# Performance work log

Hardware: AMD Instinct MI355X
Metric: run time of the kernel (lower is better)

## Reference

```python
import jax, jax.numpy as jnp
import numpy as np

WINDOW = 128
LOOK_BACKWARD = 1
LOOK_FORWARD = 1
SCALE = 64 ** -0.5  # dim_heads ** -0.5 per LocalAttention(dim=dim_heads)


def look_around(x, pad_value):
    # x: (b, w, WINDOW, ...). Pad window axis, concat shifted copies along axis 2.
    w = x.shape[1]
    pad_width = [(0, 0)] * x.ndim
    pad_width[1] = (LOOK_BACKWARD, LOOK_FORWARD)
    padded = jnp.pad(x, pad_width, constant_values=pad_value)
    return jnp.concatenate([padded[:, i:i + w] for i in range(LOOK_BACKWARD + LOOK_FORWARD + 1)], axis=2)


def setup_inputs() -> dict:
    key = jax.random.key(0)
    ks = jax.random.split(key, 8)
    B, N, D_IN, D_QK = 8, 4000, 512, 512
    return {
        "queries": jax.random.normal(ks[0], (B, N, D_IN), jnp.float32),
        "keys": jax.random.normal(ks[1], (B, N, D_IN), jnp.float32),
        "values": jax.random.normal(ks[2], (B, N, D_IN), jnp.float32),
        "mask": jax.random.bernoulli(ks[3], 0.9, (B, N)),
        "w_q": jax.random.normal(ks[4], (D_QK, D_IN), jnp.float32) / np.sqrt(D_IN).astype(np.float32),
        "b_q": jnp.zeros((D_QK,), jnp.float32),
        "w_k": jax.random.normal(ks[5], (D_QK, D_IN), jnp.float32) / np.sqrt(D_IN).astype(np.float32),
        "b_k": jnp.zeros((D_QK,), jnp.float32),
        "w_v": jax.random.normal(ks[6], (D_QK, D_IN), jnp.float32) / np.sqrt(D_IN).astype(np.float32),
        "b_v": jnp.zeros((D_QK,), jnp.float32),
    }


def local_attention(q, k, v, mask):
    b, n, d = q.shape
    pad = (-n) % WINDOW  # autopad=True
    npad = n + pad
    q = jnp.pad(q, ((0, 0), (0, pad), (0, 0)))
    k = jnp.pad(k, ((0, 0), (0, pad), (0, 0)))
    v = jnp.pad(v, ((0, 0), (0, pad), (0, 0)))
    m = jnp.pad(mask, ((0, 0), (0, pad)), constant_values=False)
    w = npad // WINDOW
    bq = q.reshape(b, w, WINDOW, d) * SCALE
    bk = look_around(k.reshape(b, w, WINDOW, d), 0.0)   # (b, w, 3W, d)
    bv = look_around(v.reshape(b, w, WINDOW, d), 0.0)
    sim = jnp.einsum('bwie,bwje->bwij', bq, bk)          # (b, w, W, 3W)
    seq = jnp.arange(npad).reshape(1, w, WINDOW)
    bq_k = look_around(seq, -1)                          # (1, w, 3W)
    pad_mask = (bq_k == -1)[:, :, None, :]
    key_mask = look_around(m.reshape(b, w, WINDOW), False)[:, :, None, :]
    neg = -jnp.finfo(sim.dtype).max
    sim = jnp.where(pad_mask | (~key_mask), neg, sim)
    attn = jax.nn.softmax(sim, axis=-1)
    out = jnp.einsum('bwij,bwje->bwie', attn, bv)
    return out.reshape(b, npad, d)[:, :n]


def reference(queries, keys, values, mask, w_q, b_q, w_k, b_k, w_v, b_v):
    q = queries @ w_q.T + b_q
    k = keys @ w_k.T + b_k
    v = values @ w_v.T + b_v
    return local_attention(q, k, v, mask)
```

## Files before the change

### kernel.cpp

```cpp
#include <hip/hip_runtime.h>
#include <cstdint>
#include <cstddef>

#define NB    8
#define NSEQ  4000
#define NPAD  4096
#define DIM   512
#define NWIN  32
#define SCALE 0.125f
#define NEG_MAX (-3.402823466e38f)

typedef _Float16 half8 __attribute__((ext_vector_type(8)));
typedef _Float16 half4 __attribute__((ext_vector_type(4)));
typedef float    floatx4 __attribute__((ext_vector_type(4)));

typedef const __attribute__((address_space(1))) void* gas_p;
typedef __attribute__((address_space(3))) void*       las_p;

__device__ __forceinline__ void gl_lds16(const void* g, void* l) {
    __builtin_amdgcn_global_load_lds((gas_p)g, (las_p)l, 16, 0, 0);
}

__global__ __launch_bounds__(256) void convert_w(
    const float* __restrict__ wq, const float* __restrict__ wk,
    const float* __restrict__ wv, _Float16* __restrict__ wh)
{
    int i = (blockIdx.x * 256 + threadIdx.x) * 4;
    floatx4 a = *(const floatx4*)(wq + i);
    half4 h;
    #pragma unroll
    for (int j = 0; j < 4; j++) h[j] = (_Float16)(a[j] * SCALE);
    *(half4*)(wh + i) = h;

    a = *(const floatx4*)(wk + i);
    #pragma unroll
    for (int j = 0; j < 4; j++) h[j] = (_Float16)a[j];
    *(half4*)(wh + 262144 + i) = h;

    a = *(const floatx4*)(wv + i);
    #pragma unroll
    for (int j = 0; j < 4; j++) h[j] = (_Float16)a[j];
    *(half4*)(wh + 524288 + i) = h;
}

__global__ __launch_bounds__(256) void proj_gemm(
    const float* __restrict__ xq, const float* __restrict__ xk,
    const float* __restrict__ xv, const _Float16* __restrict__ wh,
    const float* __restrict__ bq, const float* __restrict__ bk,
    const float* __restrict__ bv,
    _Float16* __restrict__ qh, _Float16* __restrict__ kh,
    _Float16* __restrict__ vT)
{
    const int z  = blockIdx.z;
    const int m0 = blockIdx.x * 128;
    const int n0 = blockIdx.y * 128;
    const int tid = threadIdx.x;
    const int wid = tid >> 6, lane = tid & 63;
    const int l16 = lane & 15, lg = lane >> 4;
    const int wr = wid >> 1, wc = wid & 1;

    __shared__ __align__(16) _Float16 AB[2][2][4096];

    const float* X = (z == 0) ? xq : ((z == 1) ? xk : xv);
    const _Float16* Wz = wh + (size_t)z * DIM * DIM;

    const int s0 = tid * 16;
    const int s1 = 4096 + tid * 16;
    const int k8_0 = s0 >> 11, row_0 = (s0 >> 4) & 127;
    const int k8_1 = s1 >> 11, row_1 = (s1 >> 4) & 127;
    const int ldsu0 = wid * 1024;
    const int ldsu1 = 4096 + wid * 1024;

    const float* xp0 = X + (size_t)(m0 + row_0) * DIM + k8_0 * 8;
    const float* xp1 = X + (size_t)(m0 + row_1) * DIM + k8_1 * 8;

    floatx4 acc[4][4];
    #pragma unroll
    for (int m = 0; m < 4; m++)
        #pragma unroll
        for (int n = 0; n < 4; n++) acc[m][n] = floatx4{0.f, 0.f, 0.f, 0.f};

    {
        floatx4 a0 = *(const floatx4*)(xp0);
        floatx4 a1 = *(const floatx4*)(xp0 + 4);
        floatx4 a2 = *(const floatx4*)(xp1);
        floatx4 a3 = *(const floatx4*)(xp1 + 4);
        gl_lds16(Wz + (size_t)(n0 + row_0) * DIM + k8_0 * 8, (char*)&AB[0][1][0] + ldsu0);
        gl_lds16(Wz + (size_t)(n0 + row_1) * DIM + k8_1 * 8, (char*)&AB[0][1][0] + ldsu1);
        half8 h0, h1;
        #pragma unroll
        for (int j = 0; j < 4; j++) {
            h0[j] = (_Float16)a0[j]; h0[j + 4] = (_Float16)a1[j];
            h1[j] = (_Float16)a2[j]; h1[j + 4] = (_Float16)a3[j];
        }
        *(half8*)((char*)&AB[0][0][0] + s0) = h0;
        *(half8*)((char*)&AB[0][0][0] + s1) = h1;
    }
    __syncthreads();

    for (int ks = 0; ks < 16; ks++) {
        const int cur = ks & 1;
        floatx4 a0, a1, a2, a3;
        if (ks < 15) {
            const int k0 = (ks + 1) * 32;
            a0 = *(const floatx4*)(xp0 + k0);
            a1 = *(const floatx4*)(xp0 + k0 + 4);
            a2 = *(const floatx4*)(xp1 + k0);
            a3 = *(const floatx4*)(xp1 + k0 + 4);
            gl_lds16(Wz + (size_t)(n0 + row_0) * DIM + k0 + k8_0 * 8,
                     (char*)&AB[cur ^ 1][1][0] + ldsu0);
            gl_lds16(Wz + (size_t)(n0 + row_1) * DIM + k0 + k8_1 * 8,
                     (char*)&AB[cur ^ 1][1][0] + ldsu1);
        }
        const _Float16* Ar = &AB[cur][0][lg * 1024 + (wr * 64 + l16) * 8];
        const _Float16* Br = &AB[cur][1][lg * 1024 + (wc * 64 + l16) * 8];
        half8 af[4], bf[4];
        #pragma unroll
        for (int m = 0; m < 4; m++) af[m] = *(const half8*)(Ar + m * 128);
        #pragma unroll
        for (int n = 0; n < 4; n++) bf[n] = *(const half8*)(Br + n * 128);
        #pragma unroll
        for (int m = 0; m < 4; m++)
            #pragma unroll
            for (int n = 0; n < 4; n++)
                acc[m][n] = __builtin_amdgcn_mfma_f32_16x16x32_f16(af[m], bf[n], acc[m][n], 0, 0, 0);
        if (ks < 15) {
            half8 h0, h1;
            #pragma unroll
            for (int j = 0; j < 4; j++) {
                h0[j] = (_Float16)a0[j]; h0[j + 4] = (_Float16)a1[j];
                h1[j] = (_Float16)a2[j]; h1[j + 4] = (_Float16)a3[j];
            }
            *(half8*)((char*)&AB[cur ^ 1][0][0] + s0) = h0;
            *(half8*)((char*)&AB[cur ^ 1][0][0] + s1) = h1;
            __syncthreads();
        }
    }

    const float* bias = (z == 0) ? bq : ((z == 1) ? bk : bv);
    const float bscale = (z == 0) ? SCALE : 1.0f;
    #pragma unroll
    for (int n = 0; n < 4; n++) {
        const int ncol = n0 + wc * 64 + n * 16 + l16;
        const float bn = bias[ncol] * bscale;
        #pragma unroll
        for (int m = 0; m < 4; m++) {
            const int r0 = m0 + wr * 64 + m * 16 + lg * 4;
            const int bb = r0 / NSEQ;
            const int i0 = r0 - bb * NSEQ;
            if (z < 2) {
                _Float16* O = (z == 0) ? qh : kh;
                #pragma unroll
                for (int j = 0; j < 4; j++)
                    O[((size_t)(bb * NPAD + i0 + j)) * DIM + ncol] = (_Float16)(acc[m][n][j] + bn);
            } else {
                half4 pk;
                #pragma unroll
                for (int j = 0; j < 4; j++) pk[j] = (_Float16)(acc[m][n][j] + bn);
                *(half4*)(vT + ((size_t)(bb * DIM + ncol)) * NPAD + i0) = pk;
            }
        }
    }
}

__global__ __launch_bounds__(256) void attn_scores(
    const _Float16* __restrict__ qh, const _Float16* __restrict__ kh,
    const int* __restrict__ mask, _Float16* __restrict__ P)
{
    const int h = blockIdx.x, w = blockIdx.y, b = blockIdx.z;
    const int tid = threadIdx.x;
    const int wid = tid >> 6, lane = tid & 63;
    const int l16 = lane & 15, lg = lane >> 4;

    __shared__ __align__(16) _Float16 Kl[2][12288];

    const int kbase = w * 128 - 128;
    const _Float16* khb = kh + (size_t)b * NPAD * DIM;

    int srcoff[6], ldsoff[6];
    #pragma unroll
    for (int c = 0; c < 6; c++) {
        int s = c * 4096 + tid * 16;
        int k8 = s / 6144;
        int key = (s - k8 * 6144) >> 4;
        int g = kbase + key;
        int gc = g < 0 ? 0 : (g > NPAD - 1 ? NPAD - 1 : g);
        srcoff[c] = gc * DIM + k8 * 8;
        ldsoff[c] = c * 4096 + wid * 1024;
    }

#define STAGE_K2(bb, k0) do {                                                   \
    _Pragma("unroll")                                                           \
    for (int c = 0; c < 6; c++)                                                 \
        gl_lds16(khb + (size_t)srcoff[c] + (k0), (char*)&Kl[bb][0] + ldsoff[c]);\
} while (0)

    const int qr0 = w * 128 + h * 64 + wid * 16;
    const _Float16* qrow = qh + ((size_t)(b * NPAD + qr0 + l16)) * DIM + lg * 8;

    floatx4 acc[24];
    #pragma unroll
    for (int t = 0; t < 24; t++) acc[t] = floatx4{0.f, 0.f, 0.f, 0.f};

    half8 qcur = *(const half8*)(qrow);
    STAGE_K2(0, 0);
    __syncthreads();
    for (int ks = 0; ks < 16; ks++) {
        const int cur = ks & 1;
        half8 qnext;
        if (ks < 15) {
            STAGE_K2(cur ^ 1, (ks + 1) * 32);
            qnext = *(const half8*)(qrow + (ks + 1) * 32);
        }
        const _Float16* Kb = &Kl[cur][lg * 3072 + l16 * 8];
        #pragma unroll
        for (int t = 0; t < 24; t++) {
            half8 bf = *(const half8*)(Kb + t * 128);
            acc[t] = __builtin_amdgcn_mfma_f32_16x16x32_f16(qcur, bf, acc[t], 0, 0, 0);
        }
        if (ks < 15) { __syncthreads(); qcur = qnext; }
    }
#undef STAGE_K2

    const int* mb = mask + b * NSEQ;
    #pragma unroll
    for (int t = 0; t < 24; t++) {
        int g = kbase + t * 16 + l16;
        bool keep = (g >= 0) && (g < NSEQ) && (mb[(g >= 0 && g < NSEQ) ? g : 0] != 0);
        if (!keep) acc[t] = floatx4{NEG_MAX, NEG_MAX, NEG_MAX, NEG_MAX};
    }

    _Float16* Pw = P + ((size_t)(b * NWIN + w)) * 128 * 384
                     + (size_t)(h * 64 + wid * 16) * 384;
    #pragma unroll
    for (int j = 0; j < 4; j++) {
        float mj = NEG_MAX;
        #pragma unroll
        for (int t = 0; t < 24; t++) mj = fmaxf(mj, acc[t][j]);
        mj = fmaxf(mj, __shfl_xor(mj, 1));
        mj = fmaxf(mj, __shfl_xor(mj, 2));
        mj = fmaxf(mj, __shfl_xor(mj, 4));
        mj = fmaxf(mj, __shfl_xor(mj, 8));

        float p[24];
        float lsum = 0.f;
        #pragma unroll
        for (int t = 0; t < 24; t++) { p[t] = __expf(acc[t][j] - mj); lsum += p[t]; }
        lsum += __shfl_xor(lsum, 1);
        lsum += __shfl_xor(lsum, 2);
        lsum += __shfl_xor(lsum, 4);
        lsum += __shfl_xor(lsum, 8);
        float rinv = 1.0f / lsum;

        int r = lg * 4 + j;
        #pragma unroll
        for (int t = 0; t < 24; t++)
            Pw[(size_t)r * 384 + t * 16 + l16] = (_Float16)(p[t] * rinv);
    }
}

__global__ __launch_bounds__(256) void attn_pv(
    const _Float16* __restrict__ P, const _Float16* __restrict__ vT,
    float* __restrict__ out)
{
    const int dq = blockIdx.x, w = blockIdx.y, b = blockIdx.z;
    const int tid = threadIdx.x;
    const int wid = tid >> 6, lane = tid & 63;
    const int l16 = lane & 15, lg = lane >> 4;
    const int d0 = dq * 128;

    __shared__ __align__(16) _Float16 Pl[2][4096];
    __shared__ __align__(16) _Float16 Vl[2][4096];

    const _Float16* Pw = P + ((size_t)(b * NWIN + w)) * 128 * 384;
    const _Float16* vb = vT + (size_t)b * DIM * NPAD;
    const int iw_base = w * 128 - 128;

    const int s0 = tid * 16;
    const int s1 = 4096 + tid * 16;
    const int k8_0 = s0 >> 11, row_0 = (s0 >> 4) & 127;
    const int k8_1 = s1 >> 11, row_1 = (s1 >> 4) & 127;
    const int ldsu0 = wid * 1024;
    const int ldsu1 = 4096 + wid * 1024;

#define STAGE_K3(bb, ks) do {                                                   \
    int i0 = (ks) * 32;                                                         \
    gl_lds16(Pw + (size_t)row_0 * 384 + i0 + k8_0 * 8, (char*)&Pl[bb][0] + ldsu0);\
    gl_lds16(Pw + (size_t)row_1 * 384 + i0 + k8_1 * 8, (char*)&Pl[bb][0] + ldsu1);\
    int ig0 = iw_base + i0 + k8_0 * 8;                                          \
    ig0 = ig0 < 0 ? 0 : (ig0 > NPAD - 8 ? NPAD - 8 : ig0);                      \
    int ig1 = iw_base + i0 + k8_1 * 8;                                          \
    ig1 = ig1 < 0 ? 0 : (ig1 > NPAD - 8 ? NPAD - 8 : ig1);                      \
    gl_lds16(vb + (size_t)(d0 + row_0) * NPAD + ig0, (char*)&Vl[bb][0] + ldsu0);\
    gl_lds16(vb + (size_t)(d0 + row_1) * NPAD + ig1, (char*)&Vl[bb][0] + ldsu1);\
} while (0)

    floatx4 acc[2][8];
    #pragma unroll
    for (int m = 0; m < 2; m++)
        #pragma unroll
        for (int n = 0; n < 8; n++) acc[m][n] = floatx4{0.f, 0.f, 0.f, 0.f};

    STAGE_K3(0, 0);
    __syncthreads();
    for (int ks = 0; ks < 12; ks++) {
        const int cur = ks & 1;
        if (ks < 11) STAGE_K3(cur ^ 1, ks + 1);
        const _Float16* Pr = &Pl[cur][lg * 1024 + (wid * 32 + l16) * 8];
        const _Float16* Vr = &Vl[cur][lg * 1024 + l16 * 8];
        half8 pa[2], vf[8];
        #pragma unroll
        for (int m = 0; m < 2; m++) pa[m] = *(const half8*)(Pr + m * 128);
        #pragma unroll
        for (int n = 0; n < 8; n++) vf[n] = *(const half8*)(Vr + n * 128);
        #pragma unroll
        for (int m = 0; m < 2; m++)
            #pragma unroll
            for (int n = 0; n < 8; n++)
                acc[m][n] = __builtin_amdgcn_mfma_f32_16x16x32_f16(pa[m], vf[n], acc[m][n], 0, 0, 0);
        if (ks < 11) __syncthreads();
    }
#undef STAGE_K3

    #pragma unroll
    for (int m = 0; m < 2; m++) {
        #pragma unroll
        for (int j = 0; j < 4; j++) {
            int i = w * 128 + wid * 32 + m * 16 + lg * 4 + j;
            if (i < NSEQ) {
                float* orow = out + ((size_t)b * NSEQ + i) * DIM + d0;
                #pragma unroll
                for (int n = 0; n < 8; n++) orow[n * 16 + l16] = acc[m][n][j];
            }
        }
    }
}

extern "C" void kernel_launch(void* const* d_in, const int* in_sizes, int n_in,
                              void* d_out, int out_size, void* d_ws, size_t ws_size,
                              hipStream_t stream)
{
    const float* xq = (const float*)d_in[0];
    const float* xk = (const float*)d_in[1];
    const float* xv = (const float*)d_in[2];
    const int*  msk = (const int*)d_in[3];
    const float* wq = (const float*)d_in[4];
    const float* bq = (const float*)d_in[5];
    const float* wk = (const float*)d_in[6];
    const float* bk = (const float*)d_in[7];
    const float* wv = (const float*)d_in[8];
    const float* bv = (const float*)d_in[9];

    _Float16* qh = (_Float16*)d_ws;
    _Float16* kh = qh + (size_t)NB * NPAD * DIM;
    _Float16* vT = kh + (size_t)NB * NPAD * DIM;
    _Float16* wh = vT + (size_t)NB * NPAD * DIM;
    _Float16* P  = wh + (size_t)3 * DIM * DIM;
    float* out = (float*)d_out;

    convert_w<<<dim3(256), dim3(256), 0, stream>>>(wq, wk, wv, wh);
    proj_gemm<<<dim3(250, 4, 3), dim3(256), 0, stream>>>(
        xq, xk, xv, wh, bq, bk, bv, qh, kh, vT);
    attn_scores<<<dim3(2, NWIN, NB), dim3(256), 0, stream>>>(qh, kh, msk, P);
    attn_pv<<<dim3(4, NWIN, NB), dim3(256), 0, stream>>>(P, vT, out);
}
```

Baseline: 469.8 us.

## Fuse attention scores and PV into one kernel; remap projection grid for XCD locality

Merges the score/softmax kernel and the P·V kernel into one. Probabilities now stay in LDS, written with an XOR swizzle and reused from the K staging buffer, so the global round trip through the P workspace and one launch go away. The PV stage now reads V straight from global memory with no LDS staging or double buffering, and each block computes all 512 output columns using 32 accumulators. That raises register pressure and adds uncoalesced loads. Separately, the projection GEMM grid is flattened and remapped so that consecutive block IDs across the 8 XCDs cover the same row tiles, aiming for better L2 reuse of activations.

After: 511.6 us. +8.9%, slower.

```diff
diff --git a/kernel.cpp b/kernel.cpp
--- a/kernel.cpp
+++ b/kernel.cpp
@@ -51,9 +51,14 @@
     _Float16* __restrict__ qh, _Float16* __restrict__ kh,
     _Float16* __restrict__ vT)
 {
-    const int z  = blockIdx.z;
-    const int m0 = blockIdx.x * 128;
-    const int n0 = blockIdx.y * 128;
+    const int g = blockIdx.x;
+    const int x = g & 7, s = g >> 3;
+    const int pair = x * 94 + (s >> 2);
+    if (pair >= 750) return;
+    const int z   = pair / 250;
+    const int m0  = (pair - z * 250) * 128;
+    const int n0  = (s & 3) * 128;
+
     const int tid = threadIdx.x;
     const int wid = tid >> 6, lane = tid & 63;
     const int l16 = lane & 15, lg = lane >> 4;
@@ -163,9 +168,10 @@
     }
 }
 
-__global__ __launch_bounds__(256) void attn_scores(
+__global__ __launch_bounds__(256) void attn_fused(
     const _Float16* __restrict__ qh, const _Float16* __restrict__ kh,
-    const int* __restrict__ mask, _Float16* __restrict__ P)
+    const _Float16* __restrict__ vT, const int* __restrict__ mask,
+    float* __restrict__ out)
 {
     const int h = blockIdx.x, w = blockIdx.y, b = blockIdx.z;
     const int tid = threadIdx.x;
@@ -173,6 +179,7 @@
     const int l16 = lane & 15, lg = lane >> 4;
 
     __shared__ __align__(16) _Float16 Kl[2][12288];
+    char* Ps = (char*)&Kl[0][0];
 
     const int kbase = w * 128 - 128;
     const _Float16* khb = kh + (size_t)b * NPAD * DIM;
@@ -183,8 +190,8 @@
         int s = c * 4096 + tid * 16;
         int k8 = s / 6144;
         int key = (s - k8 * 6144) >> 4;
-        int g = kbase + key;
-        int gc = g < 0 ? 0 : (g > NPAD - 1 ? NPAD - 1 : g);
+        int gk = kbase + key;
+        int gc = gk < 0 ? 0 : (gk > NPAD - 1 ? NPAD - 1 : gk);
         srcoff[c] = gc * DIM + k8 * 8;
         ldsoff[c] = c * 4096 + wid * 1024;
     }
@@ -225,13 +232,13 @@
     const int* mb = mask + b * NSEQ;
     #pragma unroll
     for (int t = 0; t < 24; t++) {
-        int g = kbase + t * 16 + l16;
-        bool keep = (g >= 0) && (g < NSEQ) && (mb[(g >= 0 && g < NSEQ) ? g : 0] != 0);
+        int gk = kbase + t * 16 + l16;
+        bool keep = (gk >= 0) && (gk < NSEQ) && (mb[(gk >= 0 && gk < NSEQ) ? gk : 0] != 0);
         if (!keep) acc[t] = floatx4{NEG_MAX, NEG_MAX, NEG_MAX, NEG_MAX};
     }
 
-    _Float16* Pw = P + ((size_t)(b * NWIN + w)) * 128 * 384
-                     + (size_t)(h * 64 + wid * 16) * 384;
+    __syncthreads();
+
     #pragma unroll
     for (int j = 0; j < 4; j++) {
         float mj = NEG_MAX;
@@ -252,86 +259,45 @@
         lsum += __shfl_xor(lsum, 8);
         float rinv = 1.0f / lsum;
 
-        int r = lg * 4 + j;
-        #pragma unroll
-        for (int t = 0; t < 24; t++)
-            Pw[(size_t)r * 384 + t * 16 + l16] = (_Float16)(p[t] * rinv);
-    }
-}
-
-__global__ __launch_bounds__(256) void attn_pv(
-    const _Float16* __restrict__ P, const _Float16* __restrict__ vT,
-    float* __restrict__ out)
-{
-    const int dq = blockIdx.x, w = blockIdx.y, b = blockIdx.z;
-    const int tid = threadIdx.x;
-    const int wid = tid >> 6, lane = tid & 63;
-    const int l16 = lane & 15, lg = lane >> 4;
-    const int d0 = dq * 128;
-
-    __shared__ __align__(16) _Float16 Pl[2][4096];
-    __shared__ __align__(16) _Float16 Vl[2][4096];
-
-    const _Float16* Pw = P + ((size_t)(b * NWIN + w)) * 128 * 384;
+        const int q = wid * 16 + lg * 4 + j;
+        const int qswz = (q & 7) << 4;
+        #pragma unroll
+        for (int t = 0; t < 24; t++) {
+            int byte = (q * 768 + (t * 16 + l16) * 2) ^ qswz;
+            *(_Float16*)(Ps + byte) = (_Float16)(p[t] * rinv);
+        }
+    }
+
+    __syncthreads();
+
     const _Float16* vb = vT + (size_t)b * DIM * NPAD;
-    const int iw_base = w * 128 - 128;
-
-    const int s0 = tid * 16;
-    const int s1 = 4096 + tid * 16;
-    const int k8_0 = s0 >> 11, row_0 = (s0 >> 4) & 127;
-    const int k8_1 = s1 >> 11, row_1 = (s1 >> 4) & 127;
-    const int ldsu0 = wid * 1024;
-    const int ldsu1 = 4096 + wid * 1024;
-
-#define STAGE_K3(bb, ks) do {                                                   \
-    int i0 = (ks) * 32;                                                         \
-    gl_lds16(Pw + (size_t)row_0 * 384 + i0 + k8_0 * 8, (char*)&Pl[bb][0] + ldsu0);\
-    gl_lds16(Pw + (size_t)row_1 * 384 + i0 + k8_1 * 8, (char*)&Pl[bb][0] + ldsu1);\
-    int ig0 = iw_base + i0 + k8_0 * 8;                                          \
-    ig0 = ig0 < 0 ? 0 : (ig0 > NPAD - 8 ? NPAD - 8 : ig0);                      \
-    int ig1 = iw_base + i0 + k8_1 * 8;                                          \
-    ig1 = ig1 < 0 ? 0 : (ig1 > NPAD - 8 ? NPAD - 8 : ig1);                      \
-    gl_lds16(vb + (size_t)(d0 + row_0) * NPAD + ig0, (char*)&Vl[bb][0] + ldsu0);\
-    gl_lds16(vb + (size_t)(d0 + row_1) * NPAD + ig1, (char*)&Vl[bb][0] + ldsu1);\
-} while (0)
-
-    floatx4 acc[2][8];
-    #pragma unroll
-    for (int m = 0; m < 2; m++)
-        #pragma unroll
-        for (int n = 0; n < 8; n++) acc[m][n] = floatx4{0.f, 0.f, 0.f, 0.f};
-
-    STAGE_K3(0, 0);
-    __syncthreads();
+    const int iw_base = kbase;
+
+    floatx4 acc2[32];
+    #pragma unroll
+    for (int t = 0; t < 32; t++) acc2[t] = floatx4{0.f, 0.f, 0.f, 0.f};
+
     for (int ks = 0; ks < 12; ks++) {
-        const int cur = ks & 1;
-        if (ks < 11) STAGE_K3(cur ^ 1, ks + 1);
-        const _Float16* Pr = &Pl[cur][lg * 1024 + (wid * 32 + l16) * 8];
-        const _Float16* Vr = &Vl[cur][lg * 1024 + l16 * 8];
-        half8 pa[2], vf[8];
-        #pragma unroll
-        for (int m = 0; m < 2; m++) pa[m] = *(const half8*)(Pr + m * 128);
-        #pragma unroll
-        for (int n = 0; n < 8; n++) vf[n] = *(const half8*)(Vr + n * 128);
-        #pragma unroll
-        for (int m = 0; m < 2; m++)
+        const int q = wid * 16 + l16;
+        const int abyte = (q * 768 + ks * 64 + lg * 16) ^ ((q & 7) << 4);
+        half8 pa = *(const half8*)(Ps + abyte);
+        int ig = iw_base + ks * 32 + lg * 8;
+        ig = ig < 0 ? 0 : (ig > NPAD - 8 ? NPAD - 8 : ig);
+        const _Float16* vrow = vb + ig;
+        #pragma unroll
+        for (int t = 0; t < 32; t++) {
+            half8 vf = *(const half8*)(vrow + (size_t)(t * 16 + l16) * NPAD);
+            acc2[t] = __builtin_amdgcn_mfma_f32_16x16x32_f16(pa, vf, acc2[t], 0, 0, 0);
+        }
+    }
+
+    #pragma unroll
+    for (int j = 0; j < 4; j++) {
+        const int i = w * 128 + h * 64 + wid * 16 + lg * 4 + j;
+        if (i < NSEQ) {
+            float* orow = out + ((size_t)b * NSEQ + i) * DIM;
             #pragma unroll
-            for (int n = 0; n < 8; n++)
-                acc[m][n] = __builtin_amdgcn_mfma_f32_16x16x32_f16(pa[m], vf[n], acc[m][n], 0, 0, 0);
-        if (ks < 11) __syncthreads();
-    }
-#undef STAGE_K3
-
-    #pragma unroll
-    for (int m = 0; m < 2; m++) {
-        #pragma unroll
-        for (int j = 0; j < 4; j++) {
-            int i = w * 128 + wid * 32 + m * 16 + lg * 4 + j;
-            if (i < NSEQ) {
-                float* orow = out + ((size_t)b * NSEQ + i) * DIM + d0;
-                #pragma unroll
-                for (int n = 0; n < 8; n++) orow[n * 16 + l16] = acc[m][n][j];
-            }
+            for (int t = 0; t < 32; t++) orow[t * 16 + l16] = acc2[t][j];
         }
     }
 }
@@ -355,12 +321,10 @@
     _Float16* kh = qh + (size_t)NB * NPAD * DIM;
     _Float16* vT = kh + (size_t)NB * NPAD * DIM;
     _Float16* wh = vT + (size_t)NB * NPAD * DIM;
-    _Float16* P  = wh + (size_t)3 * DIM * DIM;
     float* out = (float*)d_out;
 
     convert_w<<<dim3(256), dim3(256), 0, stream>>>(wq, wk, wv, wh);
-    proj_gemm<<<dim3(250, 4, 3), dim3(256), 0, stream>>>(
+    proj_gemm<<<dim3(3008), dim3(256), 0, stream>>>(
         xq, xk, xv, wh, bq, bk, bv, qh, kh, vT);
-    attn_scores<<<dim3(2, NWIN, NB), dim3(256), 0, stream>>>(qh, kh, msk, P);
-    attn_pv<<<dim3(4, NWIN, NB), dim3(256), 0, stream>>>(P, vT, out);
-}
+    attn_fused<<<dim3(2, NWIN, NB), dim3(256), 0, stream>>>(qh, kh, vT, msk, out);
+}
```

## Replace global-to-LDS direct loads with register staging and remap GEMM blocks per XCD

Applied to the files above, without the earlier changes.

All three matmul kernels drop the direct global_load_lds path. Tiles are now loaded into registers at the top of each k-step and written to the double-buffered LDS after the MFMA work, and the thread-to-row mapping is changed so consecutive threads read contiguous 16-byte chunks of a row. The projection GEMM moves to a 1D grid of 3008 blocks, remapped so that the 4 column tiles sharing one row tile land on the same XCD, aiming for better L2 reuse of the fp32 input rows. The cost is more VGPR pressure and extra ds_write instructions, plus 8 idle blocks in the padded grid.

Result: faster. 393.6 us (-16.2%).

```diff
diff --git a/kernel.cpp b/kernel.cpp
--- a/kernel.cpp
+++ b/kernel.cpp
@@ -14,13 +14,6 @@
 typedef _Float16 half4 __attribute__((ext_vector_type(4)));
 typedef float    floatx4 __attribute__((ext_vector_type(4)));
 
-typedef const __attribute__((address_space(1))) void* gas_p;
-typedef __attribute__((address_space(3))) void*       las_p;
-
-__device__ __forceinline__ void gl_lds16(const void* g, void* l) {
-    __builtin_amdgcn_global_load_lds((gas_p)g, (las_p)l, 16, 0, 0);
-}
-
 __global__ __launch_bounds__(256) void convert_w(
     const float* __restrict__ wq, const float* __restrict__ wk,
     const float* __restrict__ wv, _Float16* __restrict__ wh)
@@ -51,9 +44,14 @@
     _Float16* __restrict__ qh, _Float16* __restrict__ kh,
     _Float16* __restrict__ vT)
 {
-    const int z  = blockIdx.z;
-    const int m0 = blockIdx.x * 128;
-    const int n0 = blockIdx.y * 128;
+    const int g = blockIdx.x;
+    const int x = g & 7, s = g >> 3;
+    const int pair = x * 94 + (s >> 2);
+    if (pair >= 750) return;
+    const int z   = pair / 250;
+    const int m0  = (pair - z * 250) * 128;
+    const int n0  = (s & 3) * 128;
+
     const int tid = threadIdx.x;
     const int wid = tid >> 6, lane = tid & 63;
     const int l16 = lane & 15, lg = lane >> 4;
@@ -64,15 +62,14 @@
     const float* X = (z == 0) ? xq : ((z == 1) ? xk : xv);
     const _Float16* Wz = wh + (size_t)z * DIM * DIM;
 
-    const int s0 = tid * 16;
-    const int s1 = 4096 + tid * 16;
-    const int k8_0 = s0 >> 11, row_0 = (s0 >> 4) & 127;
-    const int k8_1 = s1 >> 11, row_1 = (s1 >> 4) & 127;
-    const int ldsu0 = wid * 1024;
-    const int ldsu1 = 4096 + wid * 1024;
-
-    const float* xp0 = X + (size_t)(m0 + row_0) * DIM + k8_0 * 8;
-    const float* xp1 = X + (size_t)(m0 + row_1) * DIM + k8_1 * 8;
+    const int srow  = tid >> 2;
+    const int chunk = tid & 3;
+    const float* xa0 = X + (size_t)(m0 + srow) * DIM + chunk * 8;
+    const float* xa1 = X + (size_t)(m0 + 64 + srow) * DIM + chunk * 8;
+    const _Float16* wb0 = Wz + (size_t)(n0 + srow) * DIM + chunk * 8;
+    const _Float16* wb1 = Wz + (size_t)(n0 + 64 + srow) * DIM + chunk * 8;
+    const int db0 = chunk * 2048 + srow * 16;
+    const int db1 = chunk * 2048 + (64 + srow) * 16;
 
     floatx4 acc[4][4];
     #pragma unroll
@@ -80,38 +77,38 @@
         #pragma unroll
         for (int n = 0; n < 4; n++) acc[m][n] = floatx4{0.f, 0.f, 0.f, 0.f};
 
-    {
-        floatx4 a0 = *(const floatx4*)(xp0);
-        floatx4 a1 = *(const floatx4*)(xp0 + 4);
-        floatx4 a2 = *(const floatx4*)(xp1);
-        floatx4 a3 = *(const floatx4*)(xp1 + 4);
-        gl_lds16(Wz + (size_t)(n0 + row_0) * DIM + k8_0 * 8, (char*)&AB[0][1][0] + ldsu0);
-        gl_lds16(Wz + (size_t)(n0 + row_1) * DIM + k8_1 * 8, (char*)&AB[0][1][0] + ldsu1);
-        half8 h0, h1;
-        #pragma unroll
-        for (int j = 0; j < 4; j++) {
-            h0[j] = (_Float16)a0[j]; h0[j + 4] = (_Float16)a1[j];
-            h1[j] = (_Float16)a2[j]; h1[j + 4] = (_Float16)a3[j];
-        }
-        *(half8*)((char*)&AB[0][0][0] + s0) = h0;
-        *(half8*)((char*)&AB[0][0][0] + s1) = h1;
-    }
+    floatx4 la0, la1, la2, la3;
+    half8 lw0, lw1;
+
+#define LOADS_K1(k0) do {                                                       \
+    la0 = *(const floatx4*)(xa0 + (k0));                                        \
+    la1 = *(const floatx4*)(xa0 + (k0) + 4);                                    \
+    la2 = *(const floatx4*)(xa1 + (k0));                                        \
+    la3 = *(const floatx4*)(xa1 + (k0) + 4);                                    \
+    lw0 = *(const half8*)(wb0 + (k0));                                          \
+    lw1 = *(const half8*)(wb1 + (k0));                                          \
+} while (0)
+
+#define WRITES_K1(bb) do {                                                      \
+    half8 h0, h1;                                                               \
+    _Pragma("unroll")                                                           \
+    for (int j = 0; j < 4; j++) {                                               \
+        h0[j] = (_Float16)la0[j]; h0[j + 4] = (_Float16)la1[j];                 \
+        h1[j] = (_Float16)la2[j]; h1[j + 4] = (_Float16)la3[j];                 \
+    }                                                                           \
+    *(half8*)((char*)&AB[bb][0][0] + db0) = h0;                                 \
+    *(half8*)((char*)&AB[bb][0][0] + db1) = h1;                                 \
+    *(half8*)((char*)&AB[bb][1][0] + db0) = lw0;                                \
+    *(half8*)((char*)&AB[bb][1][0] + db1) = lw1;                                \
+} while (0)
+
+    LOADS_K1(0);
+    WRITES_K1(0);
     __syncthreads();
 
     for (int ks = 0; ks < 16; ks++) {
         const int cur = ks & 1;
-        floatx4 a0, a1, a2, a3;
-        if (ks < 15) {
-            const int k0 = (ks + 1) * 32;
-            a0 = *(const floatx4*)(xp0 + k0);
-            a1 = *(const floatx4*)(xp0 + k0 + 4);
-            a2 = *(const floatx4*)(xp1 + k0);
-            a3 = *(const floatx4*)(xp1 + k0 + 4);
-            gl_lds16(Wz + (size_t)(n0 + row_0) * DIM + k0 + k8_0 * 8,
-                     (char*)&AB[cur ^ 1][1][0] + ldsu0);
-            gl_lds16(Wz + (size_t)(n0 + row_1) * DIM + k0 + k8_1 * 8,
-                     (char*)&AB[cur ^ 1][1][0] + ldsu1);
-        }
+        if (ks < 15) LOADS_K1((ks + 1) * 32);
         const _Float16* Ar = &AB[cur][0][lg * 1024 + (wr * 64 + l16) * 8];
         const _Float16* Br = &AB[cur][1][lg * 1024 + (wc * 64 + l16) * 8];
         half8 af[4], bf[4];
@@ -125,17 +122,12 @@
             for (int n = 0; n < 4; n++)
                 acc[m][n] = __builtin_amdgcn_mfma_f32_16x16x32_f16(af[m], bf[n], acc[m][n], 0, 0, 0);
         if (ks < 15) {
-            half8 h0, h1;
-            #pragma unroll
-            for (int j = 0; j < 4; j++) {
-                h0[j] = (_Float16)a0[j]; h0[j + 4] = (_Float16)a1[j];
-                h1[j] = (_Float16)a2[j]; h1[j + 4] = (_Float16)a3[j];
-            }
-            *(half8*)((char*)&AB[cur ^ 1][0][0] + s0) = h0;
-            *(half8*)((char*)&AB[cur ^ 1][0][0] + s1) = h1;
+            WRITES_K1(cur ^ 1);
             __syncthreads();
         }
     }
+#undef LOADS_K1
+#undef WRITES_K1
 
     const float* bias = (z == 0) ? bq : ((z == 1) ? bk : bv);
     const float bscale = (z == 0) ? SCALE : 1.0f;
@@ -177,23 +169,17 @@
     const int kbase = w * 128 - 128;
     const _Float16* khb = kh + (size_t)b * NPAD * DIM;
 
-    int srcoff[6], ldsoff[6];
+    const int srow  = tid >> 2;
+    const int chunk = tid & 3;
+    int rowoff[6], dbyte[6];
     #pragma unroll
     for (int c = 0; c < 6; c++) {
-        int s = c * 4096 + tid * 16;
-        int k8 = s / 6144;
-        int key = (s - k8 * 6144) >> 4;
-        int g = kbase + key;
-        int gc = g < 0 ? 0 : (g > NPAD - 1 ? NPAD - 1 : g);
-        srcoff[c] = gc * DIM + k8 * 8;
-        ldsoff[c] = c * 4096 + wid * 1024;
-    }
-
-#define STAGE_K2(bb, k0) do {                                                   \
-    _Pragma("unroll")                                                           \
-    for (int c = 0; c < 6; c++)                                                 \
-        gl_lds16(khb + (size_t)srcoff[c] + (k0), (char*)&Kl[bb][0] + ldsoff[c]);\
-} while (0)
+        int krow = c * 64 + srow;
+        int gk = kbase + krow;
+        int gc = gk < 0 ? 0 : (gk > NPAD - 1 ? NPAD - 1 : gk);
+        rowoff[c] = gc * DIM + chunk * 8;
+        dbyte[c]  = chunk * 6144 + krow * 16;
+    }
 
     const int qr0 = w * 128 + h * 64 + wid * 16;
     const _Float16* qrow = qh + ((size_t)(b * NPAD + qr0 + l16)) * DIM + lg * 8;
@@ -202,15 +188,22 @@
     #pragma unroll
     for (int t = 0; t < 24; t++) acc[t] = floatx4{0.f, 0.f, 0.f, 0.f};
 
+    half8 kld[6];
+    #pragma unroll
+    for (int c = 0; c < 6; c++) kld[c] = *(const half8*)(khb + rowoff[c]);
+    #pragma unroll
+    for (int c = 0; c < 6; c++) *(half8*)((char*)&Kl[0][0] + dbyte[c]) = kld[c];
     half8 qcur = *(const half8*)(qrow);
-    STAGE_K2(0, 0);
     __syncthreads();
+
     for (int ks = 0; ks < 16; ks++) {
         const int cur = ks & 1;
         half8 qnext;
         if (ks < 15) {
-            STAGE_K2(cur ^ 1, (ks + 1) * 32);
-            qnext = *(const half8*)(qrow + (ks + 1) * 32);
+            const int k0 = (ks + 1) * 32;
+            #pragma unroll
+            for (int c = 0; c < 6; c++) kld[c] = *(const half8*)(khb + rowoff[c] + k0);
+            qnext = *(const half8*)(qrow + k0);
         }
         const _Float16* Kb = &Kl[cur][lg * 3072 + l16 * 8];
         #pragma unroll
@@ -218,15 +211,19 @@
             half8 bf = *(const half8*)(Kb + t * 128);
             acc[t] = __builtin_amdgcn_mfma_f32_16x16x32_f16(qcur, bf, acc[t], 0, 0, 0);
         }
-        if (ks < 15) { __syncthreads(); qcur = qnext; }
-    }
-#undef STAGE_K2
+        if (ks < 15) {
+            #pragma unroll
+            for (int c = 0; c < 6; c++) *(half8*)((char*)&Kl[cur ^ 1][0] + dbyte[c]) = kld[c];
+            __syncthreads();
+            qcur = qnext;
+        }
+    }
 
     const int* mb = mask + b * NSEQ;
     #pragma unroll
     for (int t = 0; t < 24; t++) {
-        int g = kbase + t * 16 + l16;
-        bool keep = (g >= 0) && (g < NSEQ) && (mb[(g >= 0 && g < NSEQ) ? g : 0] != 0);
+        int gk = kbase + t * 16 + l16;
+        bool keep = (gk >= 0) && (gk < NSEQ) && (mb[(gk >= 0 && gk < NSEQ) ? gk : 0] != 0);
         if (!keep) acc[t] = floatx4{NEG_MAX, NEG_MAX, NEG_MAX, NEG_MAX};
     }
 
@@ -276,36 +273,46 @@
     const _Float16* vb = vT + (size_t)b * DIM * NPAD;
     const int iw_base = w * 128 - 128;
 
-    const int s0 = tid * 16;
-    const int s1 = 4096 + tid * 16;
-    const int k8_0 = s0 >> 11, row_0 = (s0 >> 4) & 127;
-    const int k8_1 = s1 >> 11, row_1 = (s1 >> 4) & 127;
-    const int ldsu0 = wid * 1024;
-    const int ldsu1 = 4096 + wid * 1024;
-
-#define STAGE_K3(bb, ks) do {                                                   \
-    int i0 = (ks) * 32;                                                         \
-    gl_lds16(Pw + (size_t)row_0 * 384 + i0 + k8_0 * 8, (char*)&Pl[bb][0] + ldsu0);\
-    gl_lds16(Pw + (size_t)row_1 * 384 + i0 + k8_1 * 8, (char*)&Pl[bb][0] + ldsu1);\
-    int ig0 = iw_base + i0 + k8_0 * 8;                                          \
-    ig0 = ig0 < 0 ? 0 : (ig0 > NPAD - 8 ? NPAD - 8 : ig0);                      \
-    int ig1 = iw_base + i0 + k8_1 * 8;                                          \
-    ig1 = ig1 < 0 ? 0 : (ig1 > NPAD - 8 ? NPAD - 8 : ig1);                      \
-    gl_lds16(vb + (size_t)(d0 + row_0) * NPAD + ig0, (char*)&Vl[bb][0] + ldsu0);\
-    gl_lds16(vb + (size_t)(d0 + row_1) * NPAD + ig1, (char*)&Vl[bb][0] + ldsu1);\
+    const int srow  = tid >> 2;
+    const int chunk = tid & 3;
+    const int db0 = chunk * 2048 + srow * 16;
+    const int db1 = chunk * 2048 + (64 + srow) * 16;
+    const _Float16* pp0 = Pw + (size_t)srow * 384 + chunk * 8;
+    const _Float16* pp1 = Pw + (size_t)(64 + srow) * 384 + chunk * 8;
+    const _Float16* vv0 = vb + (size_t)(d0 + srow) * NPAD;
+    const _Float16* vv1 = vb + (size_t)(d0 + 64 + srow) * NPAD;
+
+    half8 pl0, pl1, vl0, vl1;
+
+#define LOADS_K3(ks) do {                                                       \
+    const int i0 = (ks) * 32;                                                   \
+    pl0 = *(const half8*)(pp0 + i0);                                            \
+    pl1 = *(const half8*)(pp1 + i0);                                            \
+    int ig = iw_base + i0 + chunk * 8;                                          \
+    ig = ig < 0 ? 0 : (ig > NPAD - 8 ? NPAD - 8 : ig);                          \
+    vl0 = *(const half8*)(vv0 + ig);                                            \
+    vl1 = *(const half8*)(vv1 + ig);                                            \
 } while (0)
 
+#define WRITES_K3(bb) do {                                                      \
+    *(half8*)((char*)&Pl[bb][0] + db0) = pl0;                                   \
+    *(half8*)((char*)&Pl[bb][0] + db1) = pl1;                                   \
+    *(half8*)((char*)&Vl[bb][0] + db0) = vl0;                                   \
+    *(half8*)((char*)&Vl[bb][0] + db1) = vl1;                                   \
+} while (0)
+
     floatx4 acc[2][8];
     #pragma unroll
     for (int m = 0; m < 2; m++)
         #pragma unroll
         for (int n = 0; n < 8; n++) acc[m][n] = floatx4{0.f, 0.f, 0.f, 0.f};
 
-    STAGE_K3(0, 0);
+    LOADS_K3(0);
+    WRITES_K3(0);
     __syncthreads();
     for (int ks = 0; ks < 12; ks++) {
         const int cur = ks & 1;
-        if (ks < 11) STAGE_K3(cur ^ 1, ks + 1);
+        if (ks < 11) LOADS_K3(ks + 1);
         const _Float16* Pr = &Pl[cur][lg * 1024 + (wid * 32 + l16) * 8];
         const _Float16* Vr = &Vl[cur][lg * 1024 + l16 * 8];
         half8 pa[2], vf[8];
@@ -318,9 +325,13 @@
             #pragma unroll
             for (int n = 0; n < 8; n++)
                 acc[m][n] = __builtin_amdgcn_mfma_f32_16x16x32_f16(pa[m], vf[n], acc[m][n], 0, 0, 0);
-        if (ks < 11) __syncthreads();
-    }
-#undef STAGE_K3
+        if (ks < 11) {
+            WRITES_K3(cur ^ 1);
+            __syncthreads();
+        }
+    }
+#undef LOADS_K3
+#undef WRITES_K3
 
     #pragma unroll
     for (int m = 0; m < 2; m++) {
@@ -359,7 +370,7 @@
     float* out = (float*)d_out;
 
     convert_w<<<dim3(256), dim3(256), 0, stream>>>(wq, wk, wv, wh);
-    proj_gemm<<<dim3(250, 4, 3), dim3(256), 0, stream>>>(
+    proj_gemm<<<dim3(3008), dim3(256), 0, stream>>>(
         xq, xk, xv, wh, bq, bk, bv, qh, kh, vT);
     attn_scores<<<dim3(2, NWIN, NB), dim3(256), 0, stream>>>(qh, kh, msk, P);
     attn_pv<<<dim3(4, NWIN, NB), dim3(256), 0, stream>>>(P, vT, out);
```
